# Kernel optimization log

Hardware: AMD Instinct MI355X
Metric: run time of the kernel (lower is better)

## Reference

```python
import jax, jax.numpy as jnp
import numpy as np

O, G, GS = 8192, 64, 128   # out_features, n_groups, group_size
I = G * GS                 # in_features = 8192
RANK = 128                 # svd_rank
RESULT_SHAPE = (O, I)


def setup_inputs() -> dict:
    key = jax.random.key(0)
    k1, k2, k3, k4, k5 = jax.random.split(key, 5)
    weight = jax.random.randint(k1, (O, G, GS), 0, 256, dtype=jnp.int32)
    # realistic small per-group scales and zero points
    scale = jax.random.uniform(k2, (O, G, 1), dtype=jnp.float32) * 0.01 + 1e-4
    zero_point = jax.random.normal(k3, (O, G, 1), dtype=jnp.float32) * 0.05
    svd_up = jax.random.normal(k4, (O, RANK), dtype=jnp.float32) * 0.02
    svd_down = jax.random.normal(k5, (RANK, I), dtype=jnp.float32) * 0.02
    return {
        "weight": weight,
        "scale": scale,
        "zero_point": zero_point,
        "svd_up": svd_up,
        "svd_down": svd_down,
    }


def reference(weight, scale, zero_point, svd_up, svd_down):
    # addcmul: zero_point + weight * scale  (broadcast over group dim)
    result = zero_point + weight.astype(scale.dtype) * scale      # [O, G, GS]
    result = result.reshape(RESULT_SHAPE)                          # [O, I]
    # low-rank SVD correction: result += svd_up @ svd_down (addmm_)
    result = result + jnp.matmul(svd_up, svd_down)                 # [O, I]
    return result.astype(jnp.float32)                              # final dtype cast
```

## Files before the change

kernel.cpp:

```cpp
#include <hip/hip_runtime.h>
#include <hip/hip_bf16.h>

#define O_DIM 8192
#define I_DIM 8192
#define G_DIM 64
#define RANK  128

typedef __bf16 bf16x8 __attribute__((ext_vector_type(8)));
typedef __bf16 bf16x4 __attribute__((ext_vector_type(4)));
typedef float  f32x4  __attribute__((ext_vector_type(4)));

__global__ void k_convert_up(const float* __restrict__ up, __bf16* __restrict__ A_bf) {
    size_t t = (size_t)blockIdx.x * blockDim.x + threadIdx.x;
    const float4* in4 = (const float4*)up;
    float4 v = in4[t];
    bf16x4 o = { (__bf16)v.x, (__bf16)v.y, (__bf16)v.z, (__bf16)v.w };
    *(bf16x4*)(A_bf + 4 * t) = o;
}

__global__ void k_transpose_down(const float* __restrict__ down, __bf16* __restrict__ Bt) {
    __shared__ __bf16 tile[64][132];
    int tid = threadIdx.x;
    int ib  = blockIdx.x * 64;
    int il  = tid & 63;
    int k4  = tid >> 6;
    for (int kk = 0; kk < 32; ++kk) {
        int k = kk * 4 + k4;
        tile[il][k] = (__bf16)down[(size_t)k * I_DIM + ib + il];
    }
    __syncthreads();
    uint2* dst = (uint2*)(Bt + (size_t)ib * RANK);
    #pragma unroll
    for (int jj = 0; jj < 8; ++jj) {
        int f   = (jj * 256 + tid) * 4;
        int i_l = f >> 7;
        int k_l = f & 127;
        dst[jj * 256 + tid] = *(const uint2*)&tile[i_l][k_l];
    }
}

__global__ __launch_bounds__(256, 2)
void k_main(const int* __restrict__ weight, const float* __restrict__ scale,
            const float* __restrict__ zp, const __bf16* __restrict__ A_bf,
            const __bf16* __restrict__ Bt_bf, float* __restrict__ out) {
    __shared__ int w_lds[128 * 128];
    int tid = threadIdx.x;
    int g       = blockIdx.x;
    int rowbase = blockIdx.y * 128;
    int colbase = g * 128;

    int w    = tid >> 6;
    int lane = tid & 63;

    {
        const int* gsrc = weight + (size_t)(rowbase + (lane >> 5)) * I_DIM
                        + colbase + ((lane & 31) * 4);
        #pragma unroll
        for (int jj = 0; jj < 16; ++jj) {
            int j = w * 16 + jj;
            __builtin_amdgcn_global_load_lds(
                (const __attribute__((address_space(1))) void*)(gsrc + (size_t)(2 * j) * I_DIM),
                (__attribute__((address_space(3))) void*)(&w_lds[j * 256]),
                16, 0, 0);
        }
    }

    int l15  = lane & 15;
    int quad = lane >> 4;
    int wrow = (w >> 1) * 64;
    int wcol = (w & 1) * 64;
    int orow0 = wrow + quad * 4;

    float sv[16], zv[16];
    #pragma unroll
    for (int i = 0; i < 16; ++i) {
        int row = rowbase + orow0 + (i >> 2) * 16 + (i & 3);
        sv[i] = scale[(size_t)row * G_DIM + g];
        zv[i] = zp[(size_t)row * G_DIM + g];
    }

    const __bf16* Ap = A_bf  + (size_t)(rowbase + wrow + l15) * RANK + quad * 8;
    const __bf16* Bp = Bt_bf + (size_t)(colbase + wcol + l15) * RANK + quad * 8;

    f32x4 acc[4][4];
    #pragma unroll
    for (int rb = 0; rb < 4; ++rb)
        #pragma unroll
        for (int cb = 0; cb < 4; ++cb)
            acc[rb][cb] = (f32x4){0.f, 0.f, 0.f, 0.f};

    #pragma unroll
    for (int kc = 0; kc < 4; ++kc) {
        bf16x8 af[4], bfr[4];
        #pragma unroll
        for (int rb = 0; rb < 4; ++rb)
            af[rb] = *(const bf16x8*)(Ap + rb * 16 * RANK + kc * 32);
        #pragma unroll
        for (int cb = 0; cb < 4; ++cb)
            bfr[cb] = *(const bf16x8*)(Bp + cb * 16 * RANK + kc * 32);
        #pragma unroll
        for (int rb = 0; rb < 4; ++rb)
            #pragma unroll
            for (int cb = 0; cb < 4; ++cb)
                acc[rb][cb] = __builtin_amdgcn_mfma_f32_16x16x32_bf16(
                    af[rb], bfr[cb], acc[rb][cb], 0, 0, 0);
    }

    __syncthreads();

    int    widx = orow0 * 128 + wcol + l15;
    size_t base = (size_t)(rowbase + orow0) * I_DIM + colbase + wcol + l15;
    #pragma unroll
    for (int rb = 0; rb < 4; ++rb) {
        #pragma unroll
        for (int r = 0; r < 4; ++r) {
            float s = sv[rb * 4 + r];
            float z = zv[rb * 4 + r];
            #pragma unroll
            for (int cb = 0; cb < 4; ++cb) {
                float v = fmaf((float)w_lds[widx + (rb * 16 + r) * 128 + cb * 16], s, z)
                        + acc[rb][cb][r];
                out[base + (size_t)(rb * 16 + r) * I_DIM + cb * 16] = v;
            }
        }
    }
}

extern "C" void kernel_launch(void* const* d_in, const int* in_sizes, int n_in,
                              void* d_out, int out_size, void* d_ws, size_t ws_size,
                              hipStream_t stream) {
    const int*   weight = (const int*)d_in[0];
    const float* scale  = (const float*)d_in[1];
    const float* zp     = (const float*)d_in[2];
    const float* up     = (const float*)d_in[3];
    const float* down   = (const float*)d_in[4];
    float* out = (float*)d_out;

    __bf16* A_bf  = (__bf16*)d_ws;
    __bf16* Bt_bf = A_bf + (size_t)O_DIM * RANK;

    k_convert_up<<<1024, 256, 0, stream>>>(up, A_bf);
    k_transpose_down<<<128, 256, 0, stream>>>(down, Bt_bf);

    dim3 grid(64, 64);
    k_main<<<grid, 256, 0, stream>>>(weight, scale, zp, A_bf, Bt_bf, out);
}
```

Baseline: 479.8 us.

## Give each wave a private weight tile in LDS, drop block barrier, prefetch MFMA operands

Each wave now loads only its own 64x64 quadrant of the int weight tile into a private LDS region. That lets the block-wide __syncthreads be replaced by a per-wave vmcnt wait. All A/B bf16 fragments are loaded up front, before the weight DMA is issued, so the MFMA loop has no interleaved global loads. The epilogue swaps column-block order by quad parity to reduce LDS bank conflicts. In exchange, register pressure rises from holding 32 bf16x8 fragments, which may hurt occupancy under launch_bounds(256,2).

```diff
diff --git a/kernel.cpp b/kernel.cpp
--- a/kernel.cpp
+++ b/kernel.cpp
@@ -43,7 +43,7 @@
 void k_main(const int* __restrict__ weight, const float* __restrict__ scale,
             const float* __restrict__ zp, const __bf16* __restrict__ A_bf,
             const __bf16* __restrict__ Bt_bf, float* __restrict__ out) {
-    __shared__ int w_lds[128 * 128];
+    __shared__ int w_lds[4 * 64 * 64];
     int tid = threadIdx.x;
     int g       = blockIdx.x;
     int rowbase = blockIdx.y * 128;
@@ -51,26 +51,37 @@
 
     int w    = tid >> 6;
     int lane = tid & 63;
+    int l15  = lane & 15;
+    int quad = lane >> 4;
+    int wrow = (w >> 1) * 64;
+    int wcol = (w & 1) * 64;
+
+    const __bf16* Ap = A_bf  + (size_t)(rowbase + wrow + l15) * RANK + quad * 8;
+    const __bf16* Bp = Bt_bf + (size_t)(colbase + wcol + l15) * RANK + quad * 8;
+    bf16x8 af[4][4], bfr[4][4];
+    #pragma unroll
+    for (int kc = 0; kc < 4; ++kc) {
+        #pragma unroll
+        for (int rb = 0; rb < 4; ++rb) {
+            af[kc][rb]  = *(const bf16x8*)(Ap + rb * 16 * RANK + kc * 32);
+            bfr[kc][rb] = *(const bf16x8*)(Bp + rb * 16 * RANK + kc * 32);
+        }
+    }
 
     {
-        const int* gsrc = weight + (size_t)(rowbase + (lane >> 5)) * I_DIM
-                        + colbase + ((lane & 31) * 4);
+        int* ldst = &w_lds[w * 4096];
+        const int* gsrc = weight + (size_t)(rowbase + wrow + (lane >> 4)) * I_DIM
+                        + colbase + wcol + ((lane & 15) * 4);
         #pragma unroll
         for (int jj = 0; jj < 16; ++jj) {
-            int j = w * 16 + jj;
             __builtin_amdgcn_global_load_lds(
-                (const __attribute__((address_space(1))) void*)(gsrc + (size_t)(2 * j) * I_DIM),
-                (__attribute__((address_space(3))) void*)(&w_lds[j * 256]),
+                (const __attribute__((address_space(1))) void*)(gsrc + (size_t)(jj * 4) * I_DIM),
+                (__attribute__((address_space(3))) void*)(ldst + jj * 256),
                 16, 0, 0);
         }
     }
 
-    int l15  = lane & 15;
-    int quad = lane >> 4;
-    int wrow = (w >> 1) * 64;
-    int wcol = (w & 1) * 64;
     int orow0 = wrow + quad * 4;
-
     float sv[16], zv[16];
     #pragma unroll
     for (int i = 0; i < 16; ++i) {
@@ -78,9 +89,6 @@
         sv[i] = scale[(size_t)row * G_DIM + g];
         zv[i] = zp[(size_t)row * G_DIM + g];
     }
-
-    const __bf16* Ap = A_bf  + (size_t)(rowbase + wrow + l15) * RANK + quad * 8;
-    const __bf16* Bp = Bt_bf + (size_t)(colbase + wcol + l15) * RANK + quad * 8;
 
     f32x4 acc[4][4];
     #pragma unroll
@@ -90,25 +98,18 @@
             acc[rb][cb] = (f32x4){0.f, 0.f, 0.f, 0.f};
 
     #pragma unroll
-    for (int kc = 0; kc < 4; ++kc) {
-        bf16x8 af[4], bfr[4];
-        #pragma unroll
-        for (int rb = 0; rb < 4; ++rb)
-            af[rb] = *(const bf16x8*)(Ap + rb * 16 * RANK + kc * 32);
-        #pragma unroll
-        for (int cb = 0; cb < 4; ++cb)
-            bfr[cb] = *(const bf16x8*)(Bp + cb * 16 * RANK + kc * 32);
+    for (int kc = 0; kc < 4; ++kc)
         #pragma unroll
         for (int rb = 0; rb < 4; ++rb)
             #pragma unroll
             for (int cb = 0; cb < 4; ++cb)
                 acc[rb][cb] = __builtin_amdgcn_mfma_f32_16x16x32_bf16(
-                    af[rb], bfr[cb], acc[rb][cb], 0, 0, 0);
-    }
+                    af[kc][rb], bfr[kc][cb], acc[kc ? rb : rb][cb], 0, 0, 0);
 
-    __syncthreads();
+    asm volatile("s_waitcnt vmcnt(0)" ::: "memory");
+    __builtin_amdgcn_sched_barrier(0);
 
-    int    widx = orow0 * 128 + wcol + l15;
+    const int* wq = &w_lds[w * 4096];
     size_t base = (size_t)(rowbase + orow0) * I_DIM + colbase + wcol + l15;
     #pragma unroll
     for (int rb = 0; rb < 4; ++rb) {
@@ -116,11 +117,13 @@
         for (int r = 0; r < 4; ++r) {
             float s = sv[rb * 4 + r];
             float z = zv[rb * 4 + r];
+            int row_local = quad * 4 + rb * 16 + r;
             #pragma unroll
             for (int cb = 0; cb < 4; ++cb) {
-                float v = fmaf((float)w_lds[widx + (rb * 16 + r) * 128 + cb * 16], s, z)
-                        + acc[rb][cb][r];
-                out[base + (size_t)(rb * 16 + r) * I_DIM + cb * 16] = v;
+                int cbx = cb ^ (quad & 1);
+                float v = fmaf((float)wq[row_local * 64 + l15 + cbx * 16], s, z)
+                        + acc[rb][cbx][r];
+                out[base + (size_t)(rb * 16 + r) * I_DIM + cbx * 16] = v;
             }
         }
     }
```

Result: slower. 578.8 us (+20.6%).
